# Performance work log

Hardware: AMD Instinct MI355X
Metric: run time of the kernel (lower is better)

The kernel has to match this reference:

```python
import jax, jax.numpy as jnp
import numpy as np

H = 1024; W = 1024
SPACE_SIGMA = 16.0; RANGE_SIGMA = 0.25
PAD_XY = 2; PAD_Z = 2
DIM = 5


def setup_inputs() -> dict:
    key = jax.random.key(0)
    k1, k2 = jax.random.split(key)
    features = jax.random.uniform(k1, (H, W, 3), dtype=jnp.float32)
    inp = jax.random.normal(k2, (H, W, 3), dtype=jnp.float32)
    return {"features": features, "inp": inp}


def _grid_dims(features_np):
    # Grid sizes are data-dependent in the original (TF builds them from
    # per-channel min/max); compute them host-side from concrete inputs.
    sh = int(float(H - 1) / SPACE_SIGMA) + 1 + 2 * PAD_XY
    sw = int(float(W - 1) / SPACE_SIGMA) + 1 + 2 * PAD_XY
    depths = []
    for c in range(3):
        ch = features_np[..., c]
        delta = float(ch.max() - ch.min())
        depths.append(int(delta / RANGE_SIGMA) + 1 + 2 * PAD_Z)
    return (sh, sw, depths[0], depths[1], depths[2])


def _both_indices(size, coord):
    left = jnp.clip(coord.astype(jnp.int32), 0, size - 1)
    right = jnp.clip(left + 1, 0, size - 1)
    return left, right


def _convn(data, n_iter=2):
    # Faithful port of the TF convn: separable [1,2,1]/4 pass per axis with
    # the exact same ping-pong buffer / boundary-keep / transpose behavior.
    buffer = jnp.zeros_like(data)
    perm = (1, 2, 3, 4, 0)
    for _ in range(n_iter):
        buffer, data = data, buffer
        for _ in range(DIM):
            newdata = (buffer[:-2] + buffer[2:] + 2.0 * buffer[1:-1]) / 4.0
            data = jnp.concatenate([data[:1], newdata, data[-1:]], axis=0)
            data = jnp.transpose(data, perm)
            buffer = jnp.transpose(buffer, perm)
    return data


def _filter(features, inp, dims):
    sh, sw, dr, dg, db = dims
    hw = H * W
    yy, xx = jnp.meshgrid(jnp.arange(H, dtype=jnp.float32),
                          jnp.arange(W, dtype=jnp.float32), indexing="ij")
    splat_yy = (yy / SPACE_SIGMA + 0.5).astype(jnp.int32) + PAD_XY
    splat_xx = (xx / SPACE_SIGMA + 0.5).astype(jnp.int32) + PAD_XY
    slice_yy = yy / SPACE_SIGMA + PAD_XY
    slice_xx = xx / SPACE_SIGMA + PAD_XY
    y_i, y_i2 = _both_indices(sh, slice_yy)
    x_i, x_i2 = _both_indices(sw, slice_xx)
    y_alpha = (slice_yy - y_i.astype(jnp.float32)).reshape(-1)
    x_alpha = (slice_xx - x_i.astype(jnp.float32)).reshape(-1)

    chans = []
    for c, depth in zip(range(3), (dr, dg, db)):
        v = features[..., c]
        v0 = v - jnp.min(v)
        splat_v = (v0 / RANGE_SIGMA + 0.5).astype(jnp.int32) + PAD_Z
        slice_v = v0 / RANGE_SIGMA + PAD_Z
        li, ri = _both_indices(depth, slice_v)
        alpha = (slice_v - li.astype(jnp.float32)).reshape(-1)
        chans.append((splat_v, li, ri, alpha))
    (splat_rr, r_i, r_i2, r_alpha) = chans[0]
    (splat_gg, g_i, g_i2, g_alpha) = chans[1]
    (splat_bb, b_i, b_i2, b_alpha) = chans[2]

    splat_coords = ((((splat_yy * sw + splat_xx) * dr + splat_rr) * dg
                     + splat_gg) * db + splat_bb).reshape(-1)  # [hw]

    idx_all = jnp.stack([y_i, y_i2, x_i, x_i2, r_i, r_i2,
                         g_i, g_i2, b_i, b_i2]).reshape(10, hw)
    alphas_all = jnp.stack([1.0 - y_alpha, y_alpha, 1.0 - x_alpha, x_alpha,
                            1.0 - r_alpha, r_alpha, 1.0 - g_alpha, g_alpha,
                            1.0 - b_alpha, b_alpha])  # [10, hw]

    # 32 corners of the 5-D hypercube; sel[c, d] picks left/right index per dim.
    corners = np.stack(np.meshgrid(*([np.arange(2)] * DIM), indexing="ij"),
                       axis=-1).reshape(-1, DIM)
    sel = corners + np.arange(DIM) * 2  # [32, 5]

    strides = (sw, dr, dg, db)
    coord = idx_all[sel[:, 0]]  # [32, hw]
    for d in range(1, DIM):
        coord = coord * strides[d - 1] + idx_all[sel[:, d]]
    alpha_prod = alphas_all[sel[:, 0]]  # [32, hw]
    for d in range(1, DIM):
        alpha_prod = alpha_prod * alphas_all[sel[:, d]]

    total = sh * sw * dr * dg * db

    def ch_filter(ch):
        grid = jnp.zeros((total,), jnp.float32).at[splat_coords].add(ch.reshape(-1))
        grid = _convn(grid.reshape(sh, sw, dr, dg, db))
        vals = grid.reshape(-1)[coord]  # [32, hw] multilinear gather
        return jnp.sum(alpha_prod * vals, axis=0).reshape(H, W)

    outT = jax.vmap(ch_filter)(jnp.transpose(inp, (2, 0, 1)))
    return jnp.transpose(outT, (1, 2, 0))


def reference(features, inp):
    dims = _grid_dims(np.asarray(features))
    return _filter(features, inp, dims)
```

## Files before the change

kernel.cpp:

```cpp
#include <hip/hip_runtime.h>

namespace {

constexpr int kH  = 1024;
constexpr int kW  = 1024;
constexpr int kHW = kH * kW;
constexpr int kSH = 68;
constexpr int kSW = 68;
constexpr int kD  = 8;
constexpr int kT3 = kSH * kSW * kD * kD * kD;

__global__ __launch_bounds__(256) void minmax_kernel(const float* __restrict__ feat,
                                                     float* __restrict__ part) {
    const float4* f4 = (const float4*)feat;
    int c = blockIdx.x * 256 + threadIdx.x;
    float4 q0 = f4[c * 3], q1 = f4[c * 3 + 1], q2 = f4[c * 3 + 2];
    float mn[3], mx[3];
    mn[0] = fminf(fminf(q0.x, q0.w), fminf(q1.z, q2.y));
    mx[0] = fmaxf(fmaxf(q0.x, q0.w), fmaxf(q1.z, q2.y));
    mn[1] = fminf(fminf(q0.y, q1.x), fminf(q1.w, q2.z));
    mx[1] = fmaxf(fmaxf(q0.y, q1.x), fmaxf(q1.w, q2.z));
    mn[2] = fminf(fminf(q0.z, q1.y), fminf(q2.x, q2.w));
    mx[2] = fmaxf(fmaxf(q0.z, q1.y), fmaxf(q2.x, q2.w));
    #pragma unroll
    for (int off = 32; off > 0; off >>= 1) {
        #pragma unroll
        for (int ch = 0; ch < 3; ++ch) {
            mn[ch] = fminf(mn[ch], __shfl_down(mn[ch], off, 64));
            mx[ch] = fmaxf(mx[ch], __shfl_down(mx[ch], off, 64));
        }
    }
    __shared__ float smn[4][3], smx[4][3];
    int wave = threadIdx.x >> 6;
    if ((threadIdx.x & 63) == 0) {
        #pragma unroll
        for (int ch = 0; ch < 3; ++ch) { smn[wave][ch] = mn[ch]; smx[wave][ch] = mx[ch]; }
    }
    __syncthreads();
    if (threadIdx.x == 0) {
        #pragma unroll
        for (int ch = 0; ch < 3; ++ch) {
            part[blockIdx.x * 6 + ch]     = fminf(fminf(smn[0][ch], smn[1][ch]), fminf(smn[2][ch], smn[3][ch]));
            part[blockIdx.x * 6 + 3 + ch] = fmaxf(fmaxf(smx[0][ch], smx[1][ch]), fmaxf(smx[2][ch], smx[3][ch]));
        }
    }
}

__global__ void params_kernel(const float* __restrict__ part, float* __restrict__ hdrF) {
    int t = threadIdx.x;
    float mn[3] = {1e30f, 1e30f, 1e30f};
    float mx[3] = {-1e30f, -1e30f, -1e30f};
    #pragma unroll
    for (int k = 0; k < 4; ++k) {
        int p = t + k * 256;
        #pragma unroll
        for (int c = 0; c < 3; ++c) {
            mn[c] = fminf(mn[c], part[p * 6 + c]);
            mx[c] = fmaxf(mx[c], part[p * 6 + 3 + c]);
        }
    }
    #pragma unroll
    for (int off = 32; off > 0; off >>= 1) {
        #pragma unroll
        for (int c = 0; c < 3; ++c) {
            mn[c] = fminf(mn[c], __shfl_down(mn[c], off, 64));
            mx[c] = fmaxf(mx[c], __shfl_down(mx[c], off, 64));
        }
    }
    __shared__ float smn[4][3], smx[4][3];
    int wave = t >> 6;
    if ((t & 63) == 0) {
        #pragma unroll
        for (int c = 0; c < 3; ++c) { smn[wave][c] = mn[c]; smx[wave][c] = mx[c]; }
    }
    __syncthreads();
    if (t == 0) {
        int* ip = (int*)(hdrF + 8);
        #pragma unroll
        for (int c = 0; c < 3; ++c) {
            float bmn = fminf(fminf(smn[0][c], smn[1][c]), fminf(smn[2][c], smn[3][c]));
            float bmx = fmaxf(fmaxf(smx[0][c], smx[1][c]), fmaxf(smx[2][c], smx[3][c]));
            float delta = bmx - bmn;
            int depth = (int)((double)delta / 0.25) + 1 + 4;
            if (depth > kD) depth = kD;
            if (depth < 1) depth = 1;
            hdrF[c] = bmn;
            ip[c] = depth;
        }
    }
}

__global__ __launch_bounds__(256) void splat_kernel(const float* __restrict__ feat,
                                                    const float* __restrict__ inp,
                                                    const float* __restrict__ hdrF,
                                                    float* __restrict__ grid) {
    int ix = blockIdx.x, iy = blockIdx.y;
    int y0 = (iy == 0) ? 0 : 16 * iy - 8;
    int x0 = (ix == 0) ? 0 : 16 * ix - 8;
    int h = (iy == 0 || iy == 64) ? 8 : 16;
    int w = (ix == 0 || ix == 64) ? 8 : 16;

    __shared__ float acc[3 * 512];
    __shared__ float fS[16 * 48], iS[16 * 48];
    {
        float4 z = make_float4(0.f, 0.f, 0.f, 0.f);
        float4* a4 = (float4*)acc;
        for (int i = threadIdx.x; i < 384; i += 256) a4[i] = z;
    }

    int rowVec = (w * 3) >> 2;
    int nvec = h * rowVec;
    const float4* f4 = (const float4*)(feat + ((long)y0 * kW + x0) * 3);
    const float4* i4 = (const float4*)(inp  + ((long)y0 * kW + x0) * 3);
    for (int t = threadIdx.x; t < nvec; t += 256) {
        int row = t / rowVec, q = t - row * rowVec;
        ((float4*)fS)[row * rowVec + q] = f4[row * (kW * 3 / 4) + q];
        ((float4*)iS)[row * rowVec + q] = i4[row * (kW * 3 / 4) + q];
    }
    __syncthreads();

    int t = threadIdx.x;
    int n = w * h;
    if (t < n) {
        int lx = t & (w - 1);
        int ly = (w == 16) ? (t >> 4) : (t >> 3);
        int o = (ly * w + lx) * 3;
        float v0 = fS[o + 0] - hdrF[0];
        float v1 = fS[o + 1] - hdrF[1];
        float v2 = fS[o + 2] - hdrF[2];
        int sr = (int)(v0 * 4.0f + 0.5f) + 2;
        int sg = (int)(v1 * 4.0f + 0.5f) + 2;
        int sb = (int)(v2 * 4.0f + 0.5f) + 2;
        int ciT = (sb << 6) + (sr << 3) + sg;
        atomicAdd(&acc[ciT],        iS[o + 0]);
        atomicAdd(&acc[512 + ciT],  iS[o + 1]);
        atomicAdd(&acc[1024 + ciT], iS[o + 2]);
    }
    __syncthreads();

    long base4 = ((long)((iy + 2) * kSW + (ix + 2))) << 7;
    const float4* a4 = (const float4*)acc;
    float4* g4 = (float4*)grid;
    for (int j = threadIdx.x; j < 384; j += 256) {
        int ch = j >> 7, idx = j & 127;
        g4[(long)ch * (kT3 / 4) + base4 + idx] = a4[ch * 128 + idx];
    }
}

__device__ __forceinline__ void blur_body(float* __restrict__ dst,
                                          const float* __restrict__ src,
                                          const float* __restrict__ Sv,
                                          int cx, int cy, long cbase,
                                          int dr, int dg, int db) {
    int ch = threadIdx.x >> 6;
    int rg = threadIdx.x & 63;
    int r = rg >> 3, g = rg & 7;

    const float* S = Sv + ch * 576;
    auto SV = [&](int b, int l) -> float { return S[b * 72 + l]; };
    auto gsp = [&](int ccy, int ccx, int rr, int gg, int bb) -> float {
        if (ccy < 2 || ccy > 66 || ccx < 2 || ccx > 66) return 0.0f;
        return src[(long)ch * kT3 + (((long)(ccy * kSW + ccx)) << 9) + (bb << 6) + (rr << 3) + gg];
    };

    bool gI = (g >= 1) && (g <= dg - 2);
    bool rI = (r >= 1) && (r <= dr - 2);

    float v[8];
    #pragma unroll
    for (int b = 0; b < 8; ++b) v[b] = SV(b, rg);

    int eHi = db - 1;

    auto o1_end = [&](int e) -> float {
        float Vm, Vp;
        if (gI)      { Vm = SV(e, rg - 1); Vp = SV(e, rg + 1); }
        else if (rI) { Vm = SV(e, rg - 8); Vp = SV(e, rg + 8); }
        else         { Vm = gsp(cy, cx - 1, r, g, e); Vp = gsp(cy, cx + 1, r, g, e); }
        return (Vm + Vp + 2.0f * SV(e, rg)) * 0.25f;
    };
    float o1_lo = o1_end(0);
    float o1_hi = o1_end(eHi);

    float o1[8];
    #pragma unroll
    for (int b = 0; b < 8; ++b) {
        float iv = 0.0f;
        if (b >= 1 && b <= 6) iv = ((v[b - 1] + v[b + 1]) + 2.0f * v[b]) * 0.25f;
        o1[b] = (b >= 1 && b <= db - 2) ? iv : (b == 0 ? o1_lo : (b == eHi ? o1_hi : 0.0f));
    }

    auto out1_in = [&](int r2, int g2, int e) -> float {
        int l2 = (r2 << 3) + g2;
        float C = SV(e, l2);
        float Nm, Np;
        if (g2 >= 1 && g2 <= dg - 2)      { Nm = SV(e, l2 - 1); Np = SV(e, l2 + 1); }
        else if (r2 >= 1 && r2 <= dr - 2) { Nm = SV(e, l2 - 8); Np = SV(e, l2 + 8); }
        else { Nm = gsp(cy, cx - 1, r2, g2, e); Np = gsp(cy, cx + 1, r2, g2, e); }
        return (Nm + Np + 2.0f * C) * 0.25f;
    };
    auto out1_x = [&](int cx2, int e) -> float {
        float C = gsp(cy, cx2, r, g, e);
        float Nm, Np;
        if (cx2 >= 1 && cx2 <= kSW - 2) { Nm = gsp(cy, cx2 - 1, r, g, e); Np = gsp(cy, cx2 + 1, r, g, e); }
        else                            { Nm = gsp(cy - 1, cx2, r, g, e); Np = gsp(cy + 1, cx2, r, g, e); }
        return (Nm + Np + 2.0f * C) * 0.25f;
    };
    auto o2_end = [&](int e, float o1e) -> float {
        float Xm, Xp;
        if (gI)      { Xm = out1_in(r, g - 1, e); Xp = out1_in(r, g + 1, e); }
        else if (rI) { Xm = out1_in(r - 1, g, e); Xp = out1_in(r + 1, g, e); }
        else         { Xm = out1_x(cx - 1, e);    Xp = out1_x(cx + 1, e); }
        return (Xm + Xp + 2.0f * o1e) * 0.25f;
    };
    float o2_lo = o2_end(0, o1_lo);
    float o2_hi = o2_end(eHi, o1_hi);

    float o2[8];
    #pragma unroll
    for (int b = 0; b < 8; ++b) {
        float iv = 0.0f;
        if (b >= 1 && b <= 6) iv = ((o1[b - 1] + o1[b + 1]) + 2.0f * o1[b]) * 0.25f;
        o2[b] = (b >= 1 && b <= db - 2) ? iv : (b == 0 ? o2_lo : (b == eHi ? o2_hi : 0.0f));
    }

    float* dp = dst + (long)ch * kT3 + cbase + (rg << 3);
    *(float4*)dp       = make_float4(o2[0], o2[1], o2[2], o2[3]);
    *(float4*)(dp + 4) = make_float4(o2[4], o2[5], o2[6], o2[7]);
}

__global__ __launch_bounds__(192) void blur2_kernel(float* __restrict__ dst,
                                                    const float* __restrict__ src,
                                                    const float* __restrict__ hdrF) {
    int cx = blockIdx.x + 2, cy = blockIdx.y + 2;
    const int* ip = (const int*)(hdrF + 8);
    int dr = ip[0], dg = ip[1], db = ip[2];

    __shared__ float Sv[3 * 576];
    long cbase = ((long)(cy * kSW + cx)) << 9;

    {
        const float4* g4 = (const float4*)src;
        for (int i = threadIdx.x; i < 384; i += 192) {
            int ch = i >> 7, i4 = i & 127;
            float4 q = g4[(long)ch * (kT3 / 4) + (cbase >> 2) + i4];
            int b = i4 >> 4;
            int rg = ((i4 >> 1) & 7) * 8 + (i4 & 1) * 4;
            *(float4*)&Sv[ch * 576 + b * 72 + rg] = q;
        }
    }
    __syncthreads();

    if (dr == 8 && dg == 8 && db == 8) {
        blur_body(dst, src, Sv, cx, cy, cbase, 8, 8, 8);
    } else {
        blur_body(dst, src, Sv, cx, cy, cbase, dr, dg, db);
    }
}

__global__ __launch_bounds__(256) void slice_kernel(const float* __restrict__ feat,
                                                    const float* __restrict__ hdrF,
                                                    const float* __restrict__ grid,
                                                    float* __restrict__ out) {
    __shared__ float sg[3 * 4 * 512 + 8];
    int tx = blockIdx.x, ty = blockIdx.y;

    {
        const float4* g4 = (const float4*)grid;
        float4* s4 = (float4*)sg;
        #pragma unroll
        for (int it = 0; it < 2; ++it) {
            int i = threadIdx.x + it * 256;
            int cell = i >> 7;
            int ci4 = i & 127;
            int cy = ty + 2 + (cell >> 1), cx = tx + 2 + (cell & 1);
            long cbase4 = ((long)(cy * kSW + cx)) << 7;
            #pragma unroll
            for (int ch = 0; ch < 3; ++ch)
                s4[ch * 512 + i] = g4[(long)ch * (kT3 / 4) + cbase4 + ci4];
        }
    }
    __syncthreads();

    const int* ip = (const int*)(hdrF + 8);
    int d3[3] = {ip[0], ip[1], ip[2]};
    int lx = threadIdx.x & 15, ly = threadIdx.x >> 4;
    int y = (ty << 4) + ly, x = (tx << 4) + lx;
    int p = (y << 10) + x;

    float ya = (float)ly * 0.0625f;
    float xa = (float)lx * 0.0625f;

    int li[3], ri[3];
    float al[3];
    #pragma unroll
    for (int c = 0; c < 3; ++c) {
        float v0 = feat[p * 3 + c] - hdrF[c];
        float sv = v0 * 4.0f + 2.0f;
        int l = (int)sv;
        int dm = d3[c] - 1;
        l = l < 0 ? 0 : (l > dm ? dm : l);
        int rr = l + 1 > dm ? dm : l + 1;
        li[c] = l; ri[c] = rr; al[c] = sv - (float)l;
    }

    float spw[4];
    {
        float wy[2] = {1.0f - ya, ya};
        float wx[2] = {1.0f - xa, xa};
        spw[0] = wy[0] * wx[0]; spw[1] = wy[0] * wx[1];
        spw[2] = wy[1] * wx[0]; spw[3] = wy[1] * wx[1];
    }
    int rs[2] = {li[0], ri[0]}; float wrr[2] = {1.0f - al[0], al[0]};
    int gs[2] = {li[1], ri[1]}; float wgg[2] = {1.0f - al[1], al[1]};
    int bq = li[2];
    float aeff = (ri[2] > li[2]) ? al[2] : 0.0f;

    float acc0 = 0.0f, acc1 = 0.0f, acc2 = 0.0f;
    #pragma unroll
    for (int k = 0; k < 4; ++k) {
        #pragma unroll
        for (int cr = 0; cr < 2; ++cr)
        #pragma unroll
        for (int cg = 0; cg < 2; ++cg) {
            int si = (k << 9) + (rs[cr] << 6) + (gs[cg] << 3) + bq;
            float w = spw[k] * wrr[cr] * wgg[cg];
            float a0 = sg[si],        a1 = sg[si + 1];
            float b0 = sg[2048 + si], b1 = sg[2048 + si + 1];
            float c0 = sg[4096 + si], c1 = sg[4096 + si + 1];
            acc0 += w * (a0 + aeff * (a1 - a0));
            acc1 += w * (b0 + aeff * (b1 - b0));
            acc2 += w * (c0 + aeff * (c1 - c0));
        }
    }
    out[p * 3 + 0] = acc0;
    out[p * 3 + 1] = acc1;
    out[p * 3 + 2] = acc2;
}

}

extern "C" void kernel_launch(void* const* d_in, const int* in_sizes, int n_in,
                              void* d_out, int out_size, void* d_ws, size_t ws_size,
                              hipStream_t stream) {
    const float* feat = (const float*)d_in[0];
    const float* inp  = (const float*)d_in[1];
    float* out = (float*)d_out;

    float* hdrF  = (float*)d_ws;
    float* part  = (float*)((char*)d_ws + 1024);
    float* gridA = (float*)((char*)d_ws + 32768);
    float* gridB = gridA + 3 * (size_t)kT3;

    minmax_kernel<<<1024, 256, 0, stream>>>(feat, part);
    params_kernel<<<1, 256, 0, stream>>>(part, hdrF);

    splat_kernel<<<dim3(65, 65), 256, 0, stream>>>(feat, inp, hdrF, gridA);
    blur2_kernel<<<dim3(65, 65), 192, 0, stream>>>(gridB, gridA, hdrF);
    slice_kernel<<<dim3(64, 64), 256, 0, stream>>>(feat, hdrF, gridB, out);
}
```

Baseline: 139.6 us.

## Splat a 2x2 group of spatial cells per block in the splat kernel

The splat kernel now gives each block a 32x32 pixel window covering four spatial grid cells, keeping four per-cell histograms in shared memory, and launches 33x33 blocks instead of 65x65. Pixels are read directly from global memory with strided scalar loads instead of being staged through shared memory with float4 loads. The aim is to cut block count and launch/zeroing overhead while giving each thread several pixels to process. In exchange it uses four times the shared memory per block, which lowers occupancy, and the uncoalesced scalar loads may cost bandwidth.

```diff
diff --git a/kernel.cpp b/kernel.cpp
--- a/kernel.cpp
+++ b/kernel.cpp
@@ -94,56 +94,54 @@
                                                     const float* __restrict__ inp,
                                                     const float* __restrict__ hdrF,
                                                     float* __restrict__ grid) {
-    int ix = blockIdx.x, iy = blockIdx.y;
-    int y0 = (iy == 0) ? 0 : 16 * iy - 8;
-    int x0 = (ix == 0) ? 0 : 16 * ix - 8;
-    int h = (iy == 0 || iy == 64) ? 8 : 16;
-    int w = (ix == 0 || ix == 64) ? 8 : 16;
-
-    __shared__ float acc[3 * 512];
-    __shared__ float fS[16 * 48], iS[16 * 48];
+    int gx = blockIdx.x << 1, gy = blockIdx.y << 1;
+    int x0 = 16 * gx - 8, y0 = 16 * gy - 8;
+    int xs = x0 < 0 ? 0 : x0, ys = y0 < 0 ? 0 : y0;
+    int xe = x0 + 32 > kW ? kW : x0 + 32;
+    int ye = y0 + 32 > kH ? kH : y0 + 32;
+    int wpix = xe - xs, hpix = ye - ys;
+    int npix = wpix * hpix;
+
+    __shared__ float hist[4 * 1536];
     {
         float4 z = make_float4(0.f, 0.f, 0.f, 0.f);
-        float4* a4 = (float4*)acc;
-        for (int i = threadIdx.x; i < 384; i += 256) a4[i] = z;
-    }
-
-    int rowVec = (w * 3) >> 2;
-    int nvec = h * rowVec;
-    const float4* f4 = (const float4*)(feat + ((long)y0 * kW + x0) * 3);
-    const float4* i4 = (const float4*)(inp  + ((long)y0 * kW + x0) * 3);
-    for (int t = threadIdx.x; t < nvec; t += 256) {
-        int row = t / rowVec, q = t - row * rowVec;
-        ((float4*)fS)[row * rowVec + q] = f4[row * (kW * 3 / 4) + q];
-        ((float4*)iS)[row * rowVec + q] = i4[row * (kW * 3 / 4) + q];
-    }
-    __syncthreads();
-
-    int t = threadIdx.x;
-    int n = w * h;
-    if (t < n) {
-        int lx = t & (w - 1);
-        int ly = (w == 16) ? (t >> 4) : (t >> 3);
-        int o = (ly * w + lx) * 3;
-        float v0 = fS[o + 0] - hdrF[0];
-        float v1 = fS[o + 1] - hdrF[1];
-        float v2 = fS[o + 2] - hdrF[2];
-        int sr = (int)(v0 * 4.0f + 0.5f) + 2;
-        int sg = (int)(v1 * 4.0f + 0.5f) + 2;
-        int sb = (int)(v2 * 4.0f + 0.5f) + 2;
+        float4* h4 = (float4*)hist;
+        for (int i = threadIdx.x; i < 1536; i += 256) h4[i] = z;
+    }
+    float m0 = hdrF[0], m1 = hdrF[1], m2 = hdrF[2];
+    __syncthreads();
+
+    for (int idx = threadIdx.x; idx < npix; idx += 256) {
+        int py, px;
+        if (wpix == 32) { py = idx >> 5; px = idx & 31; }
+        else            { py = idx / wpix; px = idx - py * wpix; }
+        int X = xs + px, Y = ys + py;
+        long p = (((long)Y << 10) + X) * 3;
+        float f0 = feat[p], f1 = feat[p + 1], f2 = feat[p + 2];
+        float v0 = inp[p],  v1 = inp[p + 1],  v2 = inp[p + 2];
+        int sr = (int)((f0 - m0) * 4.0f + 0.5f) + 2;
+        int sg = (int)((f1 - m1) * 4.0f + 0.5f) + 2;
+        int sb = (int)((f2 - m2) * 4.0f + 0.5f) + 2;
+        int cl = ((((Y + 8) >> 4) - gy) << 1) + (((X + 8) >> 4) - gx);
         int ciT = (sb << 6) + (sr << 3) + sg;
-        atomicAdd(&acc[ciT],        iS[o + 0]);
-        atomicAdd(&acc[512 + ciT],  iS[o + 1]);
-        atomicAdd(&acc[1024 + ciT], iS[o + 2]);
-    }
-    __syncthreads();
-
-    long base4 = ((long)((iy + 2) * kSW + (ix + 2))) << 7;
-    const float4* a4 = (const float4*)acc;
+        float* hc = hist + cl * 1536;
+        atomicAdd(&hc[ciT],        v0);
+        atomicAdd(&hc[512 + ciT],  v1);
+        atomicAdd(&hc[1024 + ciT], v2);
+    }
+    __syncthreads();
+
+    const float4* h4 = (const float4*)hist;
     float4* g4 = (float4*)grid;
-    for (int j = threadIdx.x; j < 384; j += 256) {
-        int ch = j >> 7, idx = j & 127;
-        g4[(long)ch * (kT3 / 4) + base4 + idx] = a4[ch * 128 + idx];
+    #pragma unroll
+    for (int cl = 0; cl < 4; ++cl) {
+        int cix = gx + (cl & 1), ciy = gy + (cl >> 1);
+        if (cix > 64 || ciy > 64) continue;
+        long base4 = ((long)((ciy + 2) * kSW + (cix + 2))) << 7;
+        for (int j = threadIdx.x; j < 384; j += 256) {
+            int ch = j >> 7, id = j & 127;
+            g4[(long)ch * (kT3 / 4) + base4 + id] = h4[cl * 384 + ch * 128 + id];
+        }
     }
 }
 
@@ -355,7 +353,7 @@
     minmax_kernel<<<1024, 256, 0, stream>>>(feat, part);
     params_kernel<<<1, 256, 0, stream>>>(part, hdrF);
 
-    splat_kernel<<<dim3(65, 65), 256, 0, stream>>>(feat, inp, hdrF, gridA);
+    splat_kernel<<<dim3(33, 33), 256, 0, stream>>>(feat, inp, hdrF, gridA);
     blur2_kernel<<<dim3(65, 65), 192, 0, stream>>>(gridB, gridA, hdrF);
     slice_kernel<<<dim3(64, 64), 256, 0, stream>>>(feat, hdrF, gridB, out);
 }
```

After: 140.7 us. No clear change (+0.7%).
